# Kernel tuning notes

Measured on AMD Instinct MI355X. Metric: run time of the kernel, lower is better.

## Reference

```python
import jax, jax.numpy as jnp
import numpy as np

HIDDEN = 1024
ATTN = 1024
B, S = 4, 2048


def setup_inputs() -> dict:
    key = jax.random.key(0)
    ks = jax.random.split(key, 6)
    bound = 1.0 / np.sqrt(HIDDEN)
    return {
        "query": jax.random.normal(ks[0], (B, S, HIDDEN), jnp.float32),
        "value": jax.random.normal(ks[1], (B, S, HIDDEN), jnp.float32),
        "Wq": jax.random.uniform(ks[2], (HIDDEN, ATTN), jnp.float32, -bound, bound),
        "bq": jax.random.uniform(ks[3], (ATTN,), jnp.float32, -bound, bound),
        "Wv": jax.random.uniform(ks[4], (HIDDEN, ATTN), jnp.float32, -bound, bound),
        "bv": jax.random.uniform(ks[5], (ATTN,), jnp.float32, -bound, bound),
    }


def reference(query, value, Wq, bq, Wv, bv):
    # Linear projections (torch Linear: x @ W^T + b; here W stored as [in, out])
    q = jnp.einsum("bsh,hd->bsd", query, Wq) + bq  # [B,S,ATTN]
    v = jnp.einsum("bsh,hd->bsd", value, Wv) + bv  # [B,S,ATTN]
    # Unscaled dot-product attention
    scores = jnp.einsum("bqd,bkd->bqk", q, v)       # [B,S,S]
    attn = jax.nn.softmax(scores, axis=-1)
    context = jnp.einsum("bqk,bkd->bqd", attn, v)   # [B,S,ATTN]
    return context
```

## Files before the change

kernel.cpp:

```cpp
#include <hip/hip_runtime.h>
#include <hip/hip_bf16.h>


typedef unsigned short u16;
typedef __attribute__((ext_vector_type(8))) short bf16x8;
typedef __attribute__((ext_vector_type(4))) float f32x4;

typedef __attribute__((address_space(1))) void gvoid_t;
typedef __attribute__((address_space(3))) void svoid_t;

__device__ __forceinline__ void gll16(const void* g, void* l) {
    __builtin_amdgcn_global_load_lds((gvoid_t*)g, (svoid_t*)l, 16, 0, 0);
}

__device__ __forceinline__ u16 bf16rn(float x) {
    unsigned u = __float_as_uint(x);
    unsigned r = (u + 0x7FFFu + ((u >> 16) & 1u)) >> 16;
    return (u16)r;
}
__device__ __forceinline__ float bf2f(u16 h) {
    return __uint_as_float(((unsigned)h) << 16);
}

__device__ __forceinline__ const char* sel3(const char* p0, const char* p1,
                                            const char* p2, int i) {
    return i == 0 ? p0 : (i == 1 ? p1 : p2);
}

#define NSK 48

#define STAGE_A(T, mh) {                                                      \
    const char* _p = sel3(A0z, A1z, A2z, (T) >> 4) + (long)((T) & 15) * 128;  \
    char* _d = smem + (((T) & 1) << 16) + ((mh) << 14) + (w << 10);           \
    gll16(_p + offA##mh##0, _d);                                              \
    gll16(_p + offA##mh##1, _d + 8192); }

#define STAGE_B(T, nh) {                                                      \
    const char* _p = sel3(B0z, B1z, B2z, (T) >> 4) + (long)((T) & 15) * 128;  \
    char* _d = smem + (((T) & 1) << 16) + 32768 + ((nh) << 14) + (w << 10);   \
    gll16(_p + offB##nh##0, _d);                                              \
    gll16(_p + offB##nh##1, _d + 8192); }

#define VM4 { asm volatile("s_waitcnt vmcnt(4)" ::: "memory");                \
              __builtin_amdgcn_sched_barrier(0); }
#define VM0 { asm volatile("s_waitcnt vmcnt(0)" ::: "memory");                \
              __builtin_amdgcn_sched_barrier(0); }

#define RD_A(mh)                                                              \
    _Pragma("unroll") for (int mi = 0; mi < 4; ++mi)                          \
      _Pragma("unroll") for (int ks = 0; ks < 2; ++ks)                        \
        afr[mi][ks] = *(const bf16x8*)(smem + bufb + ((mh) << 14) +           \
            aRdB + mi * 2048 + csw[ks]);

#define RD_B(BFR, nh)                                                         \
    _Pragma("unroll") for (int ni = 0; ni < 2; ++ni)                          \
      _Pragma("unroll") for (int ks = 0; ks < 2; ++ks)                        \
        BFR[ni][ks] = *(const bf16x8*)(smem + bufb + ((nh) << 14) +           \
            bRdB + ni * 2048 + csw[ks]);

#define MFMA_Q(mh, nh, BFR) {                                                 \
    __builtin_amdgcn_s_setprio(1);                                            \
    _Pragma("unroll") for (int mi = 0; mi < 4; ++mi)                          \
      _Pragma("unroll") for (int ni = 0; ni < 2; ++ni)                        \
        _Pragma("unroll") for (int ks = 0; ks < 2; ++ks)                      \
          acc[(mh) * 4 + mi][(nh) * 2 + ni] =                                 \
              __builtin_amdgcn_mfma_f32_16x16x32_bf16(                        \
                  afr[mi][ks], BFR[ni][ks],                                   \
                  acc[(mh) * 4 + mi][(nh) * 2 + ni], 0, 0, 0);                \
    __builtin_amdgcn_s_setprio(0); }

template<bool OUTF32, int SCHEME>
__global__ __launch_bounds__(512, 2)
void gemm8(const char* a0, const char* a1, const char* a2, long zA,
           const char* b0, const char* b1, const char* b2, long zB,
           float* __restrict__ Of, u16* __restrict__ Ohi, u16* __restrict__ Olo,
           long zC, const float* __restrict__ bias0,
           const float* __restrict__ bias1, int N)
{
    extern __shared__ char smem[];
    const int t = threadIdx.x, lane = t & 63, w = t >> 6;
    const int wm = w >> 2, wn = w & 3;

    const int bid = blockIdx.x;
    const int xcd = bid & 7, bi = bid >> 3;
    int m0, n0, z;
    if (SCHEME == 0) {
        z = xcd >> 1;
        m0 = (((xcd & 1) << 2) | (bi >> 3)) << 8;
        n0 = (bi & 7) << 8;
    } else {
        m0 = ((xcd << 2) | (bi >> 3)) << 8;
        n0 = (bi & 3) << 8;
        z = (bi >> 2) & 1;
    }

    const char* A0z = a0 + (long)z * zA;
    const char* A1z = a1 + (long)z * zA;
    const char* A2z = a2 + (long)z * zA;
    const char* B0z = b0 + (long)z * zB;
    const char* B1z = b1 + (long)z * zB;
    const char* B2z = b2 + (long)z * zB;

    const int lr0 = t >> 3;
    const long cg = (long)((((t & 7) ^ ((t >> 3) & 7)) << 4));
    const long offA00 = (long)(m0 + lr0) * 2048 + cg;
    const long offA01 = offA00 + 128L * 2048;
    const long offA10 = (long)(m0 + 64 + lr0) * 2048 + cg;
    const long offA11 = offA10 + 128L * 2048;
    const long offB00 = (long)(n0 + ((lr0 >> 5) << 6) + (lr0 & 31)) * 2048 + cg;
    const long offB01 = offB00 + 128L * 2048;
    const long offB10 = offB00 + 32L * 2048;
    const long offB11 = offB10 + 128L * 2048;

    const int swl = (lane & 7) << 4;
    const int csw[2] = { (((lane >> 4) << 4)) ^ swl,
                         (((lane >> 4) << 4) + 64) ^ swl };
    const int aRdB = (wm * 64 + (lane & 15)) * 128;
    const int bRdB = 32768 + (wn * 32 + (lane & 15)) * 128;

    f32x4 acc[8][4];
#pragma unroll
    for (int i = 0; i < 8; ++i)
#pragma unroll
        for (int j = 0; j < 4; ++j) acc[i][j] = (f32x4)0.f;
    bf16x8 afr[4][2];
    bf16x8 b0r[2][2], b1r[2][2];

    STAGE_A(0, 0); STAGE_B(0, 0); STAGE_A(0, 1); STAGE_B(0, 1);
    STAGE_A(1, 0); STAGE_B(1, 0);
    asm volatile("s_waitcnt vmcnt(4)" ::: "memory");
    __builtin_amdgcn_sched_barrier(0);
    __builtin_amdgcn_s_barrier();

    for (int s = 0; s < NSK - 2; ++s) {
        const int bufb = (s & 1) << 16;
        RD_A(0); RD_B(b0r, 0);
        STAGE_A(s + 1, 1);
        MFMA_Q(0, 0, b0r);
        RD_B(b1r, 1);
        STAGE_B(s + 1, 1);
        MFMA_Q(0, 1, b1r);
        __builtin_amdgcn_s_barrier();
        RD_A(1);
        STAGE_A(s + 2, 0);
        MFMA_Q(1, 0, b0r);
        STAGE_B(s + 2, 0);
        MFMA_Q(1, 1, b1r);
        VM4;
        __builtin_amdgcn_s_barrier();
    }
    {
        const int bufb = ((NSK - 2) & 1) << 16;
        RD_A(0); RD_B(b0r, 0);
        STAGE_A(NSK - 1, 1);
        MFMA_Q(0, 0, b0r);
        RD_B(b1r, 1);
        STAGE_B(NSK - 1, 1);
        MFMA_Q(0, 1, b1r);
        RD_A(1);
        MFMA_Q(1, 0, b0r);
        MFMA_Q(1, 1, b1r);
        VM0;
        __builtin_amdgcn_s_barrier();
    }
    {
        const int bufb = ((NSK - 1) & 1) << 16;
        RD_A(0); RD_B(b0r, 0);
        MFMA_Q(0, 0, b0r);
        RD_B(b1r, 1);
        MFMA_Q(0, 1, b1r);
        RD_A(1);
        MFMA_Q(1, 0, b0r);
        MFMA_Q(1, 1, b1r);
    }

    const int r0 = m0 + wm * 128 + ((lane >> 4) << 2);
    const int c0 = n0 + wn * 64 + (lane & 15);
    if (OUTF32) {
        float* Co = Of + (long)z * zC;
#pragma unroll
        for (int mi = 0; mi < 8; ++mi)
#pragma unroll
            for (int nj = 0; nj < 4; ++nj)
#pragma unroll
                for (int r = 0; r < 4; ++r)
                    Co[(long)(r0 + mi * 16 + r) * N + c0 + nj * 16] =
                        acc[mi][nj][r];
    } else {
        const float* bs = z ? bias1 : bias0;
        float bc[4];
#pragma unroll
        for (int nj = 0; nj < 4; ++nj) bc[nj] = bs[c0 + nj * 16];
        u16* Oh = Ohi + (long)z * zC;
        u16* Ol = Olo + (long)z * zC;
#pragma unroll
        for (int mi = 0; mi < 8; ++mi)
#pragma unroll
            for (int nj = 0; nj < 4; ++nj)
#pragma unroll
                for (int r = 0; r < 4; ++r) {
                    float x = acc[mi][nj][r] + bc[nj];
                    long o = (long)(r0 + mi * 16 + r) * N + c0 + nj * 16;
                    u16 h = bf16rn(x);
                    Oh[o] = h;
                    Ol[o] = bf16rn(x - bf2f(h));
                }
    }
}

#define PVNSK 64

#define PV_STAGE_A(T, mh) {                                                   \
    const char* _p = Ap + (long)((T) & 31) * 128;                             \
    char* _d = smem + (((T) & 1) * 49152) + ((mh) << 14) + (w << 10);         \
    gll16(_p + offA##mh##0, _d);                                              \
    gll16(_p + offA##mh##1, _d + 8192); }

#define PV_STAGE_B(T, nh) {                                                   \
    const char* _p = (((T) >> 5) ? Bl : Bh) + (long)((T) & 31) * 128;         \
    char* _d = smem + (((T) & 1) * 49152) + 32768 + ((nh) << 13) + (w << 10); \
    gll16(_p + offB##nh, _d); }

#define PVM3 { asm volatile("s_waitcnt vmcnt(3)" ::: "memory");               \
               __builtin_amdgcn_sched_barrier(0); }

#define PV_RD_A(mh)                                                           \
    _Pragma("unroll") for (int mi = 0; mi < 4; ++mi)                          \
      _Pragma("unroll") for (int ks = 0; ks < 2; ++ks)                        \
        afr[mi][ks] = *(const bf16x8*)(smem + bufb + ((mh) << 14) +           \
            aRdB + mi * 2048 + csw[ks]);

#define PV_RD_B(BFR, nh)                                                      \
    _Pragma("unroll") for (int ks = 0; ks < 2; ++ks)                          \
      BFR[ks] = *(const bf16x8*)(smem + bufb + 32768 + ((nh) << 13) +         \
          bRdB + csw[ks]);

#define PV_MFMA_Q(mh, nh, BFR) {                                              \
    __builtin_amdgcn_s_setprio(1);                                            \
    _Pragma("unroll") for (int mi = 0; mi < 4; ++mi)                          \
      _Pragma("unroll") for (int ks = 0; ks < 2; ++ks)                        \
        acc[(mh) * 4 + mi][nh] =                                              \
            __builtin_amdgcn_mfma_f32_16x16x32_bf16(                          \
                afr[mi][ks], BFR[ks], acc[(mh) * 4 + mi][nh], 0, 0, 0);       \
    __builtin_amdgcn_s_setprio(0); }

__global__ __launch_bounds__(512, 2)
void gemm8pv(const char* pA, const char* vTh, const char* vTl,
             float* __restrict__ Of)
{
    extern __shared__ char smem[];
    const int t = threadIdx.x, lane = t & 63, w = t >> 6;
    const int wm = w >> 2, wn = w & 3;

    const int bid = blockIdx.x;
    const int xcd = bid & 7, bi = bid >> 3;
    const int z  = xcd >> 1;
    const int m0 = ((((xcd & 1) << 2) | (bi >> 3)) << 8);
    const int n0 = (bi & 7) << 7;

    const char* Ap = pA  + (long)z * 8388608;
    const char* Bh = vTh + (long)z * 4194304;
    const char* Bl = vTl + (long)z * 4194304;

    const int lr0 = t >> 3;
    const long cg = (long)((((t & 7) ^ ((t >> 3) & 7)) << 4));
    const long offA00 = (long)(m0 + lr0) * 4096 + cg;
    const long offA01 = offA00 + 64L * 4096;
    const long offA10 = (long)(m0 + 128 + lr0) * 4096 + cg;
    const long offA11 = offA10 + 64L * 4096;
    const long offB0  = (long)(n0 + lr0) * 4096 + cg;
    const long offB1  = (long)(n0 + 64 + lr0) * 4096 + cg;

    const int swl = (lane & 7) << 4;
    const int csw[2] = { (((lane >> 4) << 4)) ^ swl,
                         (((lane >> 4) << 4) + 64) ^ swl };
    const int aRdB = (wm * 64 + (lane & 15)) * 128;
    const int bRdB = (wn * 16 + (lane & 15)) * 128;

    f32x4 acc[8][2];
#pragma unroll
    for (int i = 0; i < 8; ++i) { acc[i][0] = (f32x4)0.f; acc[i][1] = (f32x4)0.f; }
    bf16x8 afr[4][2];
    bf16x8 bA[2], bB[2];

    PV_STAGE_A(0, 0); PV_STAGE_B(0, 0); PV_STAGE_A(0, 1); PV_STAGE_B(0, 1);
    PV_STAGE_A(1, 0); PV_STAGE_B(1, 0);
    asm volatile("s_waitcnt vmcnt(3)" ::: "memory");
    __builtin_amdgcn_sched_barrier(0);
    __builtin_amdgcn_s_barrier();

    for (int s = 0; s < PVNSK - 2; ++s) {
        const int bufb = (s & 1) * 49152;
        PV_RD_A(0); PV_RD_B(bA, 0);
        PV_STAGE_A(s + 1, 1);
        PV_MFMA_Q(0, 0, bA);
        PV_RD_B(bB, 1);
        PV_STAGE_B(s + 1, 1);
        PV_MFMA_Q(0, 1, bB);
        __builtin_amdgcn_s_barrier();
        PV_RD_A(1);
        PV_STAGE_A(s + 2, 0);
        PV_MFMA_Q(1, 0, bA);
        PV_STAGE_B(s + 2, 0);
        PV_MFMA_Q(1, 1, bB);
        PVM3;
        __builtin_amdgcn_s_barrier();
    }
    {
        const int bufb = ((PVNSK - 2) & 1) * 49152;
        PV_RD_A(0); PV_RD_B(bA, 0);
        PV_STAGE_A(PVNSK - 1, 1);
        PV_MFMA_Q(0, 0, bA);
        PV_RD_B(bB, 1);
        PV_STAGE_B(PVNSK - 1, 1);
        PV_MFMA_Q(0, 1, bB);
        PV_RD_A(1);
        PV_MFMA_Q(1, 0, bA);
        PV_MFMA_Q(1, 1, bB);
        VM0;
        __builtin_amdgcn_s_barrier();
    }
    {
        const int bufb = ((PVNSK - 1) & 1) * 49152;
        PV_RD_A(0); PV_RD_B(bA, 0);
        PV_MFMA_Q(0, 0, bA);
        PV_RD_B(bB, 1);
        PV_MFMA_Q(0, 1, bB);
        PV_RD_A(1);
        PV_MFMA_Q(1, 0, bA);
        PV_MFMA_Q(1, 1, bB);
    }

    float* Co = Of + (long)z * 2097152;
    const int r0 = m0 + wm * 64 + ((lane >> 4) << 2);
    const int c0 = n0 + wn * 16 + (lane & 15);
#pragma unroll
    for (int mh = 0; mh < 2; ++mh)
#pragma unroll
        for (int mi = 0; mi < 4; ++mi)
#pragma unroll
            for (int nh = 0; nh < 2; ++nh)
#pragma unroll
                for (int r = 0; r < 4; ++r)
                    Co[(long)(r0 + mh * 128 + mi * 16 + r) * 1024 +
                       c0 + nh * 64] = acc[mh * 4 + mi][nh][r];
}

__global__ __launch_bounds__(256)
void split2_f32(const float* __restrict__ q, const float* __restrict__ v,
                u16* __restrict__ qh, u16* __restrict__ ql,
                u16* __restrict__ vh, u16* __restrict__ vl)
{
    const int sel = blockIdx.y;
    const float* in = sel ? v : q;
    u16* hi = sel ? vh : qh;
    u16* lo = sel ? vl : ql;
    long i = ((long)blockIdx.x * 256 + threadIdx.x) * 4;
    float4 x = *(const float4*)(in + i);
    ushort4 h, l;
    h.x = bf16rn(x.x); l.x = bf16rn(x.x - bf2f(h.x));
    h.y = bf16rn(x.y); l.y = bf16rn(x.y - bf2f(h.y));
    h.z = bf16rn(x.z); l.z = bf16rn(x.z - bf2f(h.z));
    h.w = bf16rn(x.w); l.w = bf16rn(x.w - bf2f(h.w));
    *(ushort4*)(hi + i) = h;
    *(ushort4*)(lo + i) = l;
}

__global__ __launch_bounds__(256)
void tsplit2_w(const float* __restrict__ Wq, const float* __restrict__ Wv,
               u16* __restrict__ qhi, u16* __restrict__ qlo,
               u16* __restrict__ vhi, u16* __restrict__ vlo)
{
    __shared__ float tile[32][33];
    const int sel = blockIdx.z;
    const float* W = sel ? Wv : Wq;
    u16* hi = sel ? vhi : qhi;
    u16* lo = sel ? vlo : qlo;
    const int n0v = blockIdx.x * 32, k0 = blockIdx.y * 32;
    const int r = threadIdx.x >> 5, c = threadIdx.x & 31;
#pragma unroll
    for (int it = 0; it < 4; ++it)
        tile[r + it * 8][c] = W[(long)(k0 + r + it * 8) * 1024 + n0v + c];
    __syncthreads();
#pragma unroll
    for (int it = 0; it < 4; ++it) {
        const int rr = r + it * 8;
        float x = tile[c][rr];
        u16 h = bf16rn(x);
        long o = (long)(n0v + rr) * 1024 + k0 + c;
        hi[o] = h;
        lo[o] = bf16rn(x - bf2f(h));
    }
}

__global__ __launch_bounds__(256)
void tr2_bf16(const u16* __restrict__ v_hi, const u16* __restrict__ v_lo,
              u16* __restrict__ vT_hi, u16* __restrict__ vT_lo)
{
    __shared__ u16 tile[64][68];
    const int pl = blockIdx.z & 1, b = blockIdx.z >> 1;
    const u16* src = (pl ? v_lo : v_hi) + (long)b * 2097152;
    u16* dst = (pl ? vT_lo : vT_hi) + (long)b * 2097152;
    const int s0 = blockIdx.x * 64, d0 = blockIdx.y * 64;
    const int t = threadIdx.x;
    const int rr = t >> 4, c4 = (t & 15) * 4;
#pragma unroll
    for (int it = 0; it < 4; ++it) {
        const int s = it * 16 + rr;
        *(short4*)&tile[s][c4] =
            *(const short4*)(src + (long)(s0 + s) * 1024 + d0 + c4);
    }
    __syncthreads();
#pragma unroll
    for (int it = 0; it < 4; ++it) {
        const int d = it * 16 + rr;
        short4 o;
        o.x = tile[c4 + 0][d]; o.y = tile[c4 + 1][d];
        o.z = tile[c4 + 2][d]; o.w = tile[c4 + 3][d];
        *(short4*)(dst + (long)(d0 + d) * 2048 + s0 + c4) = o;
    }
}

__global__ __launch_bounds__(256)
void softmax_p(const float* __restrict__ S, u16* __restrict__ P)
{
    const float* p = S + (long)blockIdx.x * 2048;
    u16* o = P + (long)blockIdx.x * 2048;
    const int t = threadIdx.x;

    float4 x0 = *(const float4*)&p[t * 4];
    float4 x1 = *(const float4*)&p[1024 + t * 4];

    float mx = fmaxf(fmaxf(fmaxf(x0.x, x0.y), fmaxf(x0.z, x0.w)),
                     fmaxf(fmaxf(x1.x, x1.y), fmaxf(x1.z, x1.w)));
#pragma unroll
    for (int off = 32; off; off >>= 1) mx = fmaxf(mx, __shfl_xor(mx, off));

    __shared__ float red[8];
    if ((t & 63) == 0) red[t >> 6] = mx;
    __syncthreads();
    mx = fmaxf(fmaxf(red[0], red[1]), fmaxf(red[2], red[3]));

    x0.x = __expf(x0.x - mx); x0.y = __expf(x0.y - mx);
    x0.z = __expf(x0.z - mx); x0.w = __expf(x0.w - mx);
    x1.x = __expf(x1.x - mx); x1.y = __expf(x1.y - mx);
    x1.z = __expf(x1.z - mx); x1.w = __expf(x1.w - mx);

    float sm2 = (x0.x + x0.y + x0.z + x0.w) + (x1.x + x1.y + x1.z + x1.w);
#pragma unroll
    for (int off = 32; off; off >>= 1) sm2 += __shfl_xor(sm2, off);
    if ((t & 63) == 0) red[4 + (t >> 6)] = sm2;
    __syncthreads();
    sm2 = (red[4] + red[5]) + (red[6] + red[7]);

    const float inv = 1.0f / sm2;
    ushort4 y;
    y.x = bf16rn(x0.x * inv); y.y = bf16rn(x0.y * inv);
    y.z = bf16rn(x0.z * inv); y.w = bf16rn(x0.w * inv);
    *(ushort4*)(o + t * 4) = y;
    y.x = bf16rn(x1.x * inv); y.y = bf16rn(x1.y * inv);
    y.z = bf16rn(x1.z * inv); y.w = bf16rn(x1.w * inv);
    *(ushort4*)(o + 1024 + t * 4) = y;
}

extern "C" void kernel_launch(void* const* d_in, const int* in_sizes, int n_in,
                              void* d_out, int out_size, void* d_ws, size_t ws_size,
                              hipStream_t stream)
{
    const float* query = (const float*)d_in[0];
    const float* value = (const float*)d_in[1];
    const float* Wq    = (const float*)d_in[2];
    const float* bq    = (const float*)d_in[3];
    const float* Wv    = (const float*)d_in[4];
    const float* bv    = (const float*)d_in[5];
    float* out = (float*)d_out;

    char* W = (char*)d_ws;
    u16* qx_hi = (u16*)(W);
    u16* qx_lo = qx_hi + 8388608;
    u16* vx_hi = qx_lo + 8388608;
    u16* vx_lo = vx_hi + 8388608;
    float* sc  = (float*)W;
    u16* q_hi  = (u16*)(W + 67108864);
    u16* q_lo  = q_hi + 8388608;
    u16* p     = (u16*)(W + 67108864);
    u16* v_hi  = (u16*)(W + 100663296);
    u16* v_lo  = v_hi + 8388608;
    u16* vT_hi = (u16*)(W + 134217728);
    u16* vT_lo = vT_hi + 8388608;
    u16* WqT_hi = (u16*)(W + 167772160);
    u16* WqT_lo = WqT_hi + 1048576;
    u16* WvT_hi = WqT_lo + 1048576;
    u16* WvT_lo = WvT_hi + 1048576;

    hipFuncSetAttribute((const void*)&gemm8<false, 1>,
                        hipFuncAttributeMaxDynamicSharedMemorySize, 131072);
    hipFuncSetAttribute((const void*)&gemm8<true, 0>,
                        hipFuncAttributeMaxDynamicSharedMemorySize, 131072);
    hipFuncSetAttribute((const void*)&gemm8pv,
                        hipFuncAttributeMaxDynamicSharedMemorySize, 98304);

    split2_f32<<<dim3(8192, 2), 256, 0, stream>>>(query, value,
                                                  qx_hi, qx_lo, vx_hi, vx_lo);
    tsplit2_w<<<dim3(32, 32, 2), 256, 0, stream>>>(Wq, Wv,
                                                   WqT_hi, WqT_lo, WvT_hi, WvT_lo);

    gemm8<false, 1><<<256, 512, 131072, stream>>>(
        (const char*)qx_hi, (const char*)qx_hi, (const char*)qx_lo, 33554432L,
        (const char*)WqT_hi, (const char*)WqT_lo, (const char*)WqT_hi, 4194304L,
        nullptr, q_hi, q_lo, 16777216L, bq, bv, 1024);

    tr2_bf16<<<dim3(32, 16, 8), 256, 0, stream>>>(v_hi, v_lo, vT_hi, vT_lo);

    gemm8<true, 0><<<256, 512, 131072, stream>>>(
        (const char*)q_hi, (const char*)q_hi, (const char*)q_lo, 4194304L,
        (const char*)v_hi, (const char*)v_lo, (const char*)v_hi, 4194304L,
        sc, nullptr, nullptr, 4194304L, nullptr, nullptr, 2048);

    softmax_p<<<8192, 256, 0, stream>>>(sc, p);

    gemm8pv<<<256, 512, 98304, stream>>>(
        (const char*)p, (const char*)vT_hi, (const char*)vT_lo, out);
}
```

Before: 379.6 us.

## Simplify GEMM pipelines to one-stage prefetch with single barrier per k-step

Replaces the staggered two-ahead prefetch schedule in both the projection GEMM and the PV GEMM with a simpler double-buffer scheme. Each k-step now issues all loads for the next tile at the start and finishes with one wait-all and one barrier, instead of interleaving half-tile stages with partial vmcnt waits and two barriers. This cuts barrier count and scheduling complexity, but load latency is now hidden only by one k-step of MFMA work and every iteration waits for all outstanding loads.

```diff
diff --git a/kernel.cpp b/kernel.cpp
--- a/kernel.cpp
+++ b/kernel.cpp
@@ -41,8 +41,6 @@
     gll16(_p + offB##nh##0, _d);                                              \
     gll16(_p + offB##nh##1, _d + 8192); }
 
-#define VM4 { asm volatile("s_waitcnt vmcnt(4)" ::: "memory");                \
-              __builtin_amdgcn_sched_barrier(0); }
 #define VM0 { asm volatile("s_waitcnt vmcnt(0)" ::: "memory");                \
               __builtin_amdgcn_sched_barrier(0); }
 
@@ -127,35 +125,15 @@
     bf16x8 b0r[2][2], b1r[2][2];
 
     STAGE_A(0, 0); STAGE_B(0, 0); STAGE_A(0, 1); STAGE_B(0, 1);
-    STAGE_A(1, 0); STAGE_B(1, 0);
-    asm volatile("s_waitcnt vmcnt(4)" ::: "memory");
-    __builtin_amdgcn_sched_barrier(0);
+    VM0;
     __builtin_amdgcn_s_barrier();
 
-    for (int s = 0; s < NSK - 2; ++s) {
+    for (int s = 0; s < NSK - 1; ++s) {
         const int bufb = (s & 1) << 16;
-        RD_A(0); RD_B(b0r, 0);
-        STAGE_A(s + 1, 1);
+        RD_A(0); RD_B(b0r, 0); RD_B(b1r, 1);
+        STAGE_A(s + 1, 0); STAGE_B(s + 1, 0);
+        STAGE_A(s + 1, 1); STAGE_B(s + 1, 1);
         MFMA_Q(0, 0, b0r);
-        RD_B(b1r, 1);
-        STAGE_B(s + 1, 1);
-        MFMA_Q(0, 1, b1r);
-        __builtin_amdgcn_s_barrier();
-        RD_A(1);
-        STAGE_A(s + 2, 0);
-        MFMA_Q(1, 0, b0r);
-        STAGE_B(s + 2, 0);
-        MFMA_Q(1, 1, b1r);
-        VM4;
-        __builtin_amdgcn_s_barrier();
-    }
-    {
-        const int bufb = ((NSK - 2) & 1) << 16;
-        RD_A(0); RD_B(b0r, 0);
-        STAGE_A(NSK - 1, 1);
-        MFMA_Q(0, 0, b0r);
-        RD_B(b1r, 1);
-        STAGE_B(NSK - 1, 1);
         MFMA_Q(0, 1, b1r);
         RD_A(1);
         MFMA_Q(1, 0, b0r);
@@ -165,9 +143,8 @@
     }
     {
         const int bufb = ((NSK - 1) & 1) << 16;
-        RD_A(0); RD_B(b0r, 0);
+        RD_A(0); RD_B(b0r, 0); RD_B(b1r, 1);
         MFMA_Q(0, 0, b0r);
-        RD_B(b1r, 1);
         MFMA_Q(0, 1, b1r);
         RD_A(1);
         MFMA_Q(1, 0, b0r);
@@ -220,9 +197,6 @@
     const char* _p = (((T) >> 5) ? Bl : Bh) + (long)((T) & 31) * 128;         \
     char* _d = smem + (((T) & 1) * 49152) + 32768 + ((nh) << 13) + (w << 10); \
     gll16(_p + offB##nh, _d); }
-
-#define PVM3 { asm volatile("s_waitcnt vmcnt(3)" ::: "memory");               \
-               __builtin_amdgcn_sched_barrier(0); }
 
 #define PV_RD_A(mh)                                                           \
     _Pragma("unroll") for (int mi = 0; mi < 4; ++mi)                          \
@@ -284,35 +258,15 @@
     bf16x8 bA[2], bB[2];
 
     PV_STAGE_A(0, 0); PV_STAGE_B(0, 0); PV_STAGE_A(0, 1); PV_STAGE_B(0, 1);
-    PV_STAGE_A(1, 0); PV_STAGE_B(1, 0);
-    asm volatile("s_waitcnt vmcnt(3)" ::: "memory");
-    __builtin_amdgcn_sched_barrier(0);
+    VM0;
     __builtin_amdgcn_s_barrier();
 
-    for (int s = 0; s < PVNSK - 2; ++s) {
+    for (int s = 0; s < PVNSK - 1; ++s) {
         const int bufb = (s & 1) * 49152;
-        PV_RD_A(0); PV_RD_B(bA, 0);
-        PV_STAGE_A(s + 1, 1);
+        PV_RD_A(0); PV_RD_B(bA, 0); PV_RD_B(bB, 1);
+        PV_STAGE_A(s + 1, 0); PV_STAGE_B(s + 1, 0);
+        PV_STAGE_A(s + 1, 1); PV_STAGE_B(s + 1, 1);
         PV_MFMA_Q(0, 0, bA);
-        PV_RD_B(bB, 1);
-        PV_STAGE_B(s + 1, 1);
-        PV_MFMA_Q(0, 1, bB);
-        __builtin_amdgcn_s_barrier();
-        PV_RD_A(1);
-        PV_STAGE_A(s + 2, 0);
-        PV_MFMA_Q(1, 0, bA);
-        PV_STAGE_B(s + 2, 0);
-        PV_MFMA_Q(1, 1, bB);
-        PVM3;
-        __builtin_amdgcn_s_barrier();
-    }
-    {
-        const int bufb = ((PVNSK - 2) & 1) * 49152;
-        PV_RD_A(0); PV_RD_B(bA, 0);
-        PV_STAGE_A(PVNSK - 1, 1);
-        PV_MFMA_Q(0, 0, bA);
-        PV_RD_B(bB, 1);
-        PV_STAGE_B(PVNSK - 1, 1);
         PV_MFMA_Q(0, 1, bB);
         PV_RD_A(1);
         PV_MFMA_Q(1, 0, bA);
@@ -322,9 +276,8 @@
     }
     {
         const int bufb = ((PVNSK - 1) & 1) * 49152;
-        PV_RD_A(0); PV_RD_B(bA, 0);
+        PV_RD_A(0); PV_RD_B(bA, 0); PV_RD_B(bB, 1);
         PV_MFMA_Q(0, 0, bA);
-        PV_RD_B(bB, 1);
         PV_MFMA_Q(0, 1, bB);
         PV_RD_A(1);
         PV_MFMA_Q(1, 0, bA);
```

Result: slower. 396.3 us (+4.4%).
